# Optimization experiments

Hardware: AMD Instinct MI355X
Metric: run time of the kernel (lower is better)

Reference implementation:

```python
import jax, jax.numpy as jnp
import numpy as np

N_NODES = 50000
N_EDGES = 625000
F_IN = 128
HIDDEN = 128
N_CLASSES = 64


def setup_inputs() -> dict:
    key = jax.random.key(0)
    ks = jax.random.split(key, 8)
    x = jax.random.normal(ks[0], (N_NODES, F_IN), dtype=jnp.float32)
    edge_index = jax.random.randint(ks[1], (2, N_EDGES), 0, N_NODES, dtype=jnp.int64)
    # GCNConv weights (glorot-ish scale) and biases
    def glorot(k, fan_in, fan_out):
        s = jnp.sqrt(6.0 / (fan_in + fan_out))
        return jax.random.uniform(k, (fan_in, fan_out), minval=-s, maxval=s, dtype=jnp.float32)
    W1 = glorot(ks[2], F_IN, HIDDEN)
    b1 = jnp.zeros((HIDDEN,), dtype=jnp.float32)
    W2 = glorot(ks[3], HIDDEN, HIDDEN)
    b2 = jnp.zeros((HIDDEN,), dtype=jnp.float32)
    Wf = glorot(ks[4], HIDDEN, N_CLASSES)
    bf = jnp.zeros((N_CLASSES,), dtype=jnp.float32)
    return {"x": x, "edge_index": edge_index, "W1": W1, "b1": b1,
            "W2": W2, "b2": b2, "Wf": Wf, "bf": bf}


def reference(x, edge_index, W1, b1, W2, b2, Wf, bf):
    # Inference mode: AdaptiveDropout and F.dropout are identity (training=False).
    N = x.shape[0]
    loop = jnp.arange(N, dtype=edge_index.dtype)
    src = jnp.concatenate([edge_index[0], loop])  # source nodes (with self-loops)
    dst = jnp.concatenate([edge_index[1], loop])  # target nodes (with self-loops)
    # Symmetric GCN normalization: deg from edge weights scattered to targets
    deg = jax.ops.segment_sum(jnp.ones(dst.shape[0], dtype=x.dtype), dst, num_segments=N)
    dinv = jnp.where(deg > 0, jax.lax.rsqrt(deg), 0.0)
    norm = dinv[src] * dinv[dst]  # [E+N]

    def gcn(h, W, b):
        m = h @ W                      # [N, out]
        msg = m[src] * norm[:, None]   # gather + scale  [E+N, out]
        return jax.ops.segment_sum(msg, dst, num_segments=N) + b

    h = jax.nn.relu(gcn(x, W1, b1))
    h = jax.nn.relu(gcn(h, W2, b2))
    logits = gcn(h, Wf, bf)
    return jax.nn.log_softmax(logits, axis=1)
```

## Files before the change

### kernel.cpp

```cpp
#include <hip/hip_runtime.h>
#include <cstdint>
#include <cstddef>


#define WAVE 64
#define ELLW 64
#define NSH  8
#define BCAP 96
typedef _Float16 f16;
typedef f16  f16x4 __attribute__((ext_vector_type(4)));
typedef f16  f16x8 __attribute__((ext_vector_type(8)));
typedef float f32x4 __attribute__((ext_vector_type(4)));


__global__ __launch_bounds__(256) void k_prep(int4* __restrict__ cur4, int n4,
                                              const float* __restrict__ W1,
                                              const float* __restrict__ W2,
                                              const float* __restrict__ Wf,
                                              f16* __restrict__ Wt1,
                                              f16* __restrict__ Wt2,
                                              f16* __restrict__ Wtf) {
    const int gtid = blockIdx.x * 256 + threadIdx.x;
    const int gsz  = gridDim.x * 256;
    const int4 z = make_int4(0, 0, 0, 0);
    for (int i = gtid; i < n4; i += gsz) cur4[i] = z;
    for (int i = gtid; i < 40960; i += gsz) {
        if (i < 16384) {
            int n = i >> 7, k = i & 127;
            Wt1[i] = (f16)W1[k * 128 + n];
        } else if (i < 32768) {
            int j = i - 16384;
            int n = j >> 7, k = j & 127;
            Wt2[j] = (f16)W2[k * 128 + n];
        } else {
            int j = i - 32768;
            int n = j >> 7, k = j & 127;
            Wtf[j] = (f16)Wf[k * 64 + n];
        }
    }
}

__global__ void k_bucket(const int* __restrict__ src, const int* __restrict__ dst, int E,
                         int* __restrict__ cur, int* __restrict__ bsh, int N) {
    int e = blockIdx.x * blockDim.x + threadIdx.x;
    if (e >= E) return;
    int d = dst[e], s = src[e];
    if ((unsigned)d >= (unsigned)N || (unsigned)s >= (unsigned)N) return;
    int b  = d >> 4;
    int sh = blockIdx.x & (NSH - 1);
    int p  = atomicAdd(&cur[b * NSH + sh], 1);
    if (p < BCAP)
        bsh[(size_t)(b * NSH + sh) * BCAP + p] = ((d & 15) << 16) | s;
}

__global__ __launch_bounds__(256) void k_build(const int* __restrict__ cur,
                                               const int* __restrict__ bsh,
                                               int* __restrict__ ell,
                                               int* __restrict__ cnt, int N) {
    __shared__ int lcnt[16];
    __shared__ int pre[NSH + 1];
    const int b = blockIdx.x;
    const int t = threadIdx.x;
    if (t < 16) lcnt[t] = 0;
    if (t == 0) {
        int acc = 0;
#pragma unroll
        for (int s2 = 0; s2 < NSH; ++s2) {
            pre[s2] = acc;
            int c = cur[b * NSH + s2];
            acc += (c < BCAP ? c : BCAP);
        }
        pre[NSH] = acc;
    }
    __syncthreads();
    const int total = pre[NSH];
    for (int i = t; i < total; i += 256) {
        int s2 = 0;
        while (pre[s2 + 1] <= i) ++s2;
        int v   = bsh[(size_t)(b * NSH + s2) * BCAP + (i - pre[s2])];
        int ld  = v >> 16;
        int sa  = v & 0xFFFF;
        int slot = atomicAdd(&lcnt[ld], 1);
        if (slot < ELLW)
            ell[(size_t)(b * 16 + ld) * ELLW + slot] = sa;
    }
    __syncthreads();
    if (t < 16) {
        int node = b * 16 + t;
        if (node < N) cnt[node] = lcnt[t];
    }
}

template <int OUT, bool AF32>
__global__ __launch_bounds__(256) void k_gemm_mfma(const void* __restrict__ Av,
                                                   const f16* __restrict__ Wt,
                                                   const int* __restrict__ cnt,
                                                   f16* __restrict__ M,
                                                   int N) {
    constexpr int K  = 128;
    constexpr int CW = OUT / 64;
    __shared__ char smem[OUT * K * 2];
    __shared__ float dl[64];

    const int t    = threadIdx.x;
    const int w    = t >> 6;
    const int lane = t & 63;
    const int ln   = lane & 15;
    const int lh   = lane >> 4;
    const int row0 = blockIdx.x * 64;

    {
        constexpr int NCH = OUT * 16;
        for (int j = t; j < NCH; j += 256) {
            int n = j >> 4;
            uint32_t byte = (uint32_t)j * 16;
            uint32_t swz  = byte ^ (uint32_t)((n & 7) << 4);
            *(f16x8*)(smem + swz) = *(const f16x8*)&Wt[(size_t)j * 8];
        }
        if (t < 64) {
            int r = row0 + t;
            dl[t] = rsqrtf((float)(cnt[r < N ? r : (N - 1)] + 1));
        }
    }
    __syncthreads();

    f16x8 bfr[CW][4];
    const int c0 = w * CW;
#pragma unroll
    for (int c = 0; c < CW; ++c) {
        int n = (c0 + c) * 16 + ln;
#pragma unroll
        for (int q = 0; q < 4; ++q) {
            uint32_t byte = (uint32_t)(n * 256 + q * 64 + lh * 16);
            uint32_t swz  = byte ^ (uint32_t)((n & 7) << 4);
            bfr[c][q] = *(const f16x8*)(smem + swz);
        }
    }
    __syncthreads();

    f32x4 acc[4][CW];
#pragma unroll
    for (int s = 0; s < 4; ++s)
#pragma unroll
        for (int c = 0; c < CW; ++c)
            acc[s][c] = f32x4{0.f, 0.f, 0.f, 0.f};

#pragma unroll
    for (int s = 0; s < 4; ++s) {
        int m = row0 + s * 16 + ln;
        const size_t mrow = (size_t)(m < N ? m : (N - 1)) * K;
#pragma unroll
        for (int q = 0; q < 4; ++q) {
            f16x8 a;
            if constexpr (AF32) {
                const float* ap = (const float*)Av + mrow + q * 32 + lh * 8;
                float4 x0 = *(const float4*)ap;
                float4 x1 = *(const float4*)(ap + 4);
                a = f16x8{ (f16)x0.x, (f16)x0.y, (f16)x0.z, (f16)x0.w,
                           (f16)x1.x, (f16)x1.y, (f16)x1.z, (f16)x1.w };
            } else {
                a = *(const f16x8*)((const f16*)Av + mrow + q * 32 + lh * 8);
            }
#pragma unroll
            for (int c = 0; c < CW; ++c)
                acc[s][c] = __builtin_amdgcn_mfma_f32_16x16x32_f16(a, bfr[c][q], acc[s][c], 0, 0, 0);
        }
    }

    f16* ot = (f16*)smem;
#pragma unroll
    for (int s = 0; s < 4; ++s) {
#pragma unroll
        for (int c = 0; c < CW; ++c) {
            int col = (c0 + c) * 16 + ln;
#pragma unroll
            for (int r = 0; r < 4; ++r) {
                int rl = s * 16 + lh * 4 + r;
                ot[rl * OUT + col] = (f16)(acc[s][c][r] * dl[rl]);
            }
        }
    }
    __syncthreads();

    constexpr int CPR = OUT / 8;
    for (int j = t; j < 64 * CPR; j += 256) {
        int rl = j / CPR;
        if (row0 + rl < N)
            *(f16x8*)&M[(size_t)(row0 + rl) * OUT + (j % CPR) * 8] =
                *(const f16x8*)&ot[(size_t)j * 8];
    }
}

__global__ __launch_bounds__(256) void k_agg128_f16(const f16* __restrict__ M16,
                                                    const int* __restrict__ ell,
                                                    const int* __restrict__ cnt,
                                                    const float* __restrict__ bias,
                                                    f16* __restrict__ H16, int N) {
    const int lane = threadIdx.x & (WAVE - 1);
    const int sub  = lane >> 5;
    const int q    = (lane & 31) >> 4;
    const int fl   = lane & 15;
    const int fo   = fl * 8;
    const int node = blockIdx.x * 8 + ((threadIdx.x >> 6) << 1) + sub;
    if (node >= N) return;

    float a[8] = {0.f, 0.f, 0.f, 0.f, 0.f, 0.f, 0.f, 0.f};
    if (q == 0) {
        f16x8 v = *(const f16x8*)&M16[(size_t)node * 128 + fo];
#pragma unroll
        for (int i = 0; i < 8; ++i) a[i] = (float)v[i];
    }

    const int deg = cnt[node];
    const int e1  = deg < ELLW ? deg : ELLW;
    const int* erow = ell + (size_t)node * ELLW;
    for (int base = 0; base < e1; base += 16) {
        int   s[8];
        float w[8];
#pragma unroll
        for (int j = 0; j < 8; ++j) {
            int i = base + 2 * j + q;
            bool ok = i < e1;
            s[j] = erow[ok ? i : 0];
            w[j] = ok ? 1.f : 0.f;
        }
        f16x8 v[8];
#pragma unroll
        for (int j = 0; j < 8; ++j)
            v[j] = *(const f16x8*)&M16[(size_t)s[j] * 128 + fo];
#pragma unroll
        for (int j = 0; j < 8; ++j)
#pragma unroll
            for (int i = 0; i < 8; ++i)
                a[i] += w[j] * (float)v[j][i];
    }

#pragma unroll
    for (int i = 0; i < 8; ++i) a[i] += __shfl_xor(a[i], 16);

    if (q == 0) {
        const float dn = rsqrtf((float)(deg + 1));
        float4 b0 = *(const float4*)&bias[fo];
        float4 b1 = *(const float4*)&bias[fo + 4];
        f16x8 o;
        o[0] = (f16)fmaxf(a[0] * dn + b0.x, 0.f);
        o[1] = (f16)fmaxf(a[1] * dn + b0.y, 0.f);
        o[2] = (f16)fmaxf(a[2] * dn + b0.z, 0.f);
        o[3] = (f16)fmaxf(a[3] * dn + b0.w, 0.f);
        o[4] = (f16)fmaxf(a[4] * dn + b1.x, 0.f);
        o[5] = (f16)fmaxf(a[5] * dn + b1.y, 0.f);
        o[6] = (f16)fmaxf(a[6] * dn + b1.z, 0.f);
        o[7] = (f16)fmaxf(a[7] * dn + b1.w, 0.f);
        *(f16x8*)&H16[(size_t)node * 128 + fo] = o;
    }
}

__global__ __launch_bounds__(256) void k_agg64_lsm(const f16* __restrict__ M16,
                                                   const int* __restrict__ ell,
                                                   const int* __restrict__ cnt,
                                                   const float* __restrict__ bias,
                                                   float* __restrict__ Y, int N) {
    const int lane = threadIdx.x & (WAVE - 1);
    const int sub  = lane >> 5;
    const int q    = (lane & 31) >> 4;
    const int fl   = lane & 15;
    const int fo   = fl * 4;
    const int node = blockIdx.x * 8 + ((threadIdx.x >> 6) << 1) + sub;
    if (node >= N) return;

    float a[4] = {0.f, 0.f, 0.f, 0.f};
    if (q == 0) {
        f16x4 v = *(const f16x4*)&M16[(size_t)node * 64 + fo];
#pragma unroll
        for (int i = 0; i < 4; ++i) a[i] = (float)v[i];
    }

    const int deg = cnt[node];
    const int e1  = deg < ELLW ? deg : ELLW;
    const int* erow = ell + (size_t)node * ELLW;
    for (int base = 0; base < e1; base += 16) {
        int   s[8];
        float w[8];
#pragma unroll
        for (int j = 0; j < 8; ++j) {
            int i = base + 2 * j + q;
            bool ok = i < e1;
            s[j] = erow[ok ? i : 0];
            w[j] = ok ? 1.f : 0.f;
        }
        f16x4 v[8];
#pragma unroll
        for (int j = 0; j < 8; ++j)
            v[j] = *(const f16x4*)&M16[(size_t)s[j] * 64 + fo];
#pragma unroll
        for (int j = 0; j < 8; ++j)
#pragma unroll
            for (int i = 0; i < 4; ++i)
                a[i] += w[j] * (float)v[j][i];
    }

#pragma unroll
    for (int i = 0; i < 4; ++i) a[i] += __shfl_xor(a[i], 16);

    const float dn = rsqrtf((float)(deg + 1));
    float4 b = *(const float4*)&bias[fo];
    float v0 = a[0] * dn + b.x;
    float v1 = a[1] * dn + b.y;
    float v2 = a[2] * dn + b.z;
    float v3 = a[3] * dn + b.w;
    float m = fmaxf(fmaxf(v0, v1), fmaxf(v2, v3));
#pragma unroll
    for (int o = 8; o > 0; o >>= 1) m = fmaxf(m, __shfl_xor(m, o));
    float s = expf(v0 - m) + expf(v1 - m) + expf(v2 - m) + expf(v3 - m);
#pragma unroll
    for (int o = 8; o > 0; o >>= 1) s += __shfl_xor(s, o);
    if (q == 0) {
        float ls = logf(s);
        float4 o4 = make_float4(v0 - m - ls, v1 - m - ls, v2 - m - ls, v3 - m - ls);
        *(float4*)&Y[(size_t)node * 64 + fo] = o4;
    }
}


extern "C" void kernel_launch(void* const* d_in, const int* in_sizes, int n_in,
                              void* d_out, int out_size, void* d_ws, size_t ws_size,
                              hipStream_t stream) {
    const float* x  = (const float*)d_in[0];
    const int*   ei = (const int*)d_in[1];
    const float* W1 = (const float*)d_in[2];
    const float* b1 = (const float*)d_in[3];
    const float* W2 = (const float*)d_in[4];
    const float* b2 = (const float*)d_in[5];
    const float* Wf = (const float*)d_in[6];
    const float* bf = (const float*)d_in[7];
    float* out = (float*)d_out;

    const int N = in_sizes[0] / 128;
    const int E = in_sizes[1] / 2;
    const int* srcv = ei;
    const int* dstv = ei + E;

    char* ws = (char*)d_ws;
    auto alloc = [&](size_t bytes) -> void* {
        void* p = ws;
        ws += (bytes + 255) & ~(size_t)255;
        return p;
    };
    const int nbuck = (N + 15) / 16;
    int*   cur    = (int*)alloc((size_t)nbuck * NSH * 4 + 16);
    int*   bsh    = (int*)alloc((size_t)nbuck * NSH * BCAP * 4);
    int*   cnt    = (int*)alloc((size_t)N * 4);
    int*   ell    = (int*)alloc((size_t)N * ELLW * 4);
    f16*   m16    = (f16*)alloc((size_t)N * 128 * 2);
    f16*   h16    = (f16*)alloc((size_t)N * 128 * 2);
    f16*   Wt1    = (f16*)alloc(128 * 128 * 2);
    f16*   Wt2    = (f16*)alloc(128 * 128 * 2);
    f16*   Wtf    = (f16*)alloc(128 * 64 * 2);

    const int TB = 256;
    const int n4 = (nbuck * NSH + 3) / 4;

    k_prep<<<224, TB, 0, stream>>>((int4*)cur, n4, W1, W2, Wf, Wt1, Wt2, Wtf);
    k_bucket<<<(E + TB - 1) / TB, TB, 0, stream>>>(srcv, dstv, E, cur, bsh, N);
    k_build<<<nbuck, TB, 0, stream>>>(cur, bsh, ell, cnt, N);

    const int gemm_grid = (N + 63) / 64;
    const int agg_grid  = (N + 7) / 8;

    k_gemm_mfma<128, true><<<gemm_grid, 256, 0, stream>>>(x, Wt1, cnt, m16, N);
    k_agg128_f16<<<agg_grid, 256, 0, stream>>>(m16, ell, cnt, b1, h16, N);

    k_gemm_mfma<128, false><<<gemm_grid, 256, 0, stream>>>(h16, Wt2, cnt, m16, N);
    k_agg128_f16<<<agg_grid, 256, 0, stream>>>(m16, ell, cnt, b2, h16, N);

    k_gemm_mfma<64, false><<<gemm_grid, 256, 0, stream>>>(h16, Wtf, cnt, m16, N);
    k_agg64_lsm<<<agg_grid, 256, 0, stream>>>(m16, ell, cnt, bf, out, N);
}
```

Baseline: 164.7 us.

## Split 128-wide aggregation into feature-chunked blocks for L2 locality

The 128-feature aggregation kernel now splits its work by feature chunk. Each block handles 32 features (64 bytes) for 4 nodes, with one wave per node and 4 edge lanes-groups each loading f16x2. The grid is ordered chunk-major, so concurrent blocks touch only a quarter of the M16 table, which is meant to improve L2/cache hit rates on the random gathers. The cost is 4x as many ell/cnt index reads, narrow 4-byte loads instead of 16-byte loads, and an extra shuffle reduction step.

```diff
diff --git a/kernel.cpp b/kernel.cpp
--- a/kernel.cpp
+++ b/kernel.cpp
@@ -8,6 +8,7 @@
 #define NSH  8
 #define BCAP 96
 typedef _Float16 f16;
+typedef f16  f16x2 __attribute__((ext_vector_type(2)));
 typedef f16  f16x4 __attribute__((ext_vector_type(4)));
 typedef f16  f16x8 __attribute__((ext_vector_type(8)));
 typedef float f32x4 __attribute__((ext_vector_type(4)));
@@ -191,67 +192,63 @@
     }
 }
 
-__global__ __launch_bounds__(256) void k_agg128_f16(const f16* __restrict__ M16,
-                                                    const int* __restrict__ ell,
-                                                    const int* __restrict__ cnt,
-                                                    const float* __restrict__ bias,
-                                                    f16* __restrict__ H16, int N) {
-    const int lane = threadIdx.x & (WAVE - 1);
-    const int sub  = lane >> 5;
-    const int q    = (lane & 31) >> 4;
-    const int fl   = lane & 15;
-    const int fo   = fl * 8;
-    const int node = blockIdx.x * 8 + ((threadIdx.x >> 6) << 1) + sub;
+__global__ __launch_bounds__(256) void k_agg128_c(const f16* __restrict__ M16,
+                                                  const int* __restrict__ ell,
+                                                  const int* __restrict__ cnt,
+                                                  const float* __restrict__ bias,
+                                                  f16* __restrict__ H16, int N,
+                                                  int nbPer) {
+    const int chunk = blockIdx.x / nbPer;
+    const int nb    = blockIdx.x - chunk * nbPer;
+    const int wid   = threadIdx.x >> 6;
+    const int lane  = threadIdx.x & (WAVE - 1);
+    const int q     = lane >> 4;
+    const int fl    = lane & 15;
+    const int node  = nb * 4 + wid;
     if (node >= N) return;
-
-    float a[8] = {0.f, 0.f, 0.f, 0.f, 0.f, 0.f, 0.f, 0.f};
+    const int fo = chunk * 32 + fl * 2;
+
+    float a0 = 0.f, a1 = 0.f;
     if (q == 0) {
-        f16x8 v = *(const f16x8*)&M16[(size_t)node * 128 + fo];
-#pragma unroll
-        for (int i = 0; i < 8; ++i) a[i] = (float)v[i];
+        f16x2 v = *(const f16x2*)&M16[(size_t)node * 128 + fo];
+        a0 = (float)v.x; a1 = (float)v.y;
     }
 
     const int deg = cnt[node];
     const int e1  = deg < ELLW ? deg : ELLW;
     const int* erow = ell + (size_t)node * ELLW;
     for (int base = 0; base < e1; base += 16) {
-        int   s[8];
-        float w[8];
-#pragma unroll
-        for (int j = 0; j < 8; ++j) {
-            int i = base + 2 * j + q;
+        int   s[4];
+        float w[4];
+#pragma unroll
+        for (int j = 0; j < 4; ++j) {
+            int i = base + 4 * j + q;
             bool ok = i < e1;
             s[j] = erow[ok ? i : 0];
             w[j] = ok ? 1.f : 0.f;
         }
-        f16x8 v[8];
-#pragma unroll
-        for (int j = 0; j < 8; ++j)
-            v[j] = *(const f16x8*)&M16[(size_t)s[j] * 128 + fo];
-#pragma unroll
-        for (int j = 0; j < 8; ++j)
-#pragma unroll
-            for (int i = 0; i < 8; ++i)
-                a[i] += w[j] * (float)v[j][i];
-    }
-
-#pragma unroll
-    for (int i = 0; i < 8; ++i) a[i] += __shfl_xor(a[i], 16);
+        f16x2 v[4];
+#pragma unroll
+        for (int j = 0; j < 4; ++j)
+            v[j] = *(const f16x2*)&M16[(size_t)s[j] * 128 + fo];
+#pragma unroll
+        for (int j = 0; j < 4; ++j) {
+            a0 += w[j] * (float)v[j].x;
+            a1 += w[j] * (float)v[j].y;
+        }
+    }
+
+    a0 += __shfl_xor(a0, 16);
+    a0 += __shfl_xor(a0, 32);
+    a1 += __shfl_xor(a1, 16);
+    a1 += __shfl_xor(a1, 32);
 
     if (q == 0) {
         const float dn = rsqrtf((float)(deg + 1));
-        float4 b0 = *(const float4*)&bias[fo];
-        float4 b1 = *(const float4*)&bias[fo + 4];
-        f16x8 o;
-        o[0] = (f16)fmaxf(a[0] * dn + b0.x, 0.f);
-        o[1] = (f16)fmaxf(a[1] * dn + b0.y, 0.f);
-        o[2] = (f16)fmaxf(a[2] * dn + b0.z, 0.f);
-        o[3] = (f16)fmaxf(a[3] * dn + b0.w, 0.f);
-        o[4] = (f16)fmaxf(a[4] * dn + b1.x, 0.f);
-        o[5] = (f16)fmaxf(a[5] * dn + b1.y, 0.f);
-        o[6] = (f16)fmaxf(a[6] * dn + b1.z, 0.f);
-        o[7] = (f16)fmaxf(a[7] * dn + b1.w, 0.f);
-        *(f16x8*)&H16[(size_t)node * 128 + fo] = o;
+        float2 b = *(const float2*)&bias[fo];
+        f16x2 o = { (f16)fmaxf(a0 * dn + b.x, 0.f),
+                    (f16)fmaxf(a1 * dn + b.y, 0.f) };
+        *(f16x2*)&H16[(size_t)node * 128 + fo] = o;
     }
 }
 
@@ -365,14 +362,16 @@
     k_build<<<nbuck, TB, 0, stream>>>(cur, bsh, ell, cnt, N);
 
     const int gemm_grid = (N + 63) / 64;
-    const int agg_grid  = (N + 7) / 8;
+    const int nbPer     = (N + 3) / 4;
+    const int agg_grid  = 4 * nbPer;
+    const int agg64_grid = (N + 7) / 8;
 
     k_gemm_mfma<128, true><<<gemm_grid, 256, 0, stream>>>(x, Wt1, cnt, m16, N);
-    k_agg128_f16<<<agg_grid, 256, 0, stream>>>(m16, ell, cnt, b1, h16, N);
+    k_agg128_c<<<agg_grid, 256, 0, stream>>>(m16, ell, cnt, b1, h16, N, nbPer);
 
     k_gemm_mfma<128, false><<<gemm_grid, 256, 0, stream>>>(h16, Wt2, cnt, m16, N);
-    k_agg128_f16<<<agg_grid, 256, 0, stream>>>(m16, ell, cnt, b2, h16, N);
+    k_agg128_c<<<agg_grid, 256, 0, stream>>>(m16, ell, cnt, b2, h16, N, nbPer);
 
     k_gemm_mfma<64, false><<<gemm_grid, 256, 0, stream>>>(h16, Wtf, cnt, m16, N);
-    k_agg64_lsm<<<agg_grid, 256, 0, stream>>>(m16, ell, cnt, bf, out, N);
-}
+    k_agg64_lsm<<<agg64_grid, 256, 0, stream>>>(m16, ell, cnt, bf, out, N);
+}
```

Result: slower. 244.2 us (+48.3%).
